# Performance work log

Measured on AMD Instinct MI355X. Metric: run time of the kernel, lower is better.

## Reference

```python
import jax, jax.numpy as jnp
import numpy as np

N_BISECT_ITERS = 50  # entmax library default


def entmax_bisect(X, alpha, n_iter=N_BISECT_ITERS):
    """alpha-entmax over last axis via bisection (Peters & Martins 2019).
    Solves for tau s.t. sum(max((alpha-1)X - tau, 0)^(1/(alpha-1))) = 1."""
    am1 = alpha - 1.0
    inv = 1.0 / am1
    Xa = X * am1
    max_val = jnp.max(Xa, axis=-1, keepdims=True)
    d = X.shape[-1]
    tau_lo = max_val - 1.0                                   # _gp(1, alpha) = 1
    tau_hi = max_val - jnp.asarray(1.0 / d, X.dtype) ** am1  # _gp(1/d, alpha)

    def pfun(tau):
        return jnp.maximum(Xa - tau, 0.0) ** inv

    f_lo = jnp.sum(pfun(tau_lo), axis=-1, keepdims=True) - 1.0

    def body(i, carry):
        tau_lo, dm = carry
        dm = dm * 0.5
        tau_m = tau_lo + dm
        f_m = jnp.sum(pfun(tau_m), axis=-1, keepdims=True) - 1.0
        tau_lo = jnp.where(f_m * f_lo >= 0, tau_m, tau_lo)
        return (tau_lo, dm)

    tau_lo, _ = jax.lax.fori_loop(0, n_iter, body, (tau_lo, tau_hi - tau_lo))
    p = pfun(tau_lo)
    return p / jnp.sum(p, axis=-1, keepdims=True)  # ensure_sum_one


def setup_inputs() -> dict:
    master = jax.random.key(0)
    kq, kk, kv = jax.random.split(master, 3)
    B, H, S, D = 4, 16, 2048, 64
    return {
        "query": jax.random.normal(kq, (B, H, S, D), jnp.float32),
        "key": jax.random.normal(kk, (B, H, S, D), jnp.float32),
        "value": jax.random.normal(kv, (B, H, S, D), jnp.float32),
        "alpha": jnp.float32(1.5),  # canonical entmax-1.5
    }


def reference(query, key, value, alpha):
    D = query.shape[-1]
    scale = 1.0 / jnp.sqrt(jnp.asarray(D, query.dtype))
    scores = jnp.einsum('bhqd,bhkd->bhqk', query, key) * scale  # [B,H,S,S]
    p_attn = entmax_bisect(scores, alpha)
    out = jnp.einsum('bhqk,bhkd->bhqd', p_attn, value)
    return (out, p_attn)
```

## Files before the change

### kernel.cpp

```cpp
#include <hip/hip_runtime.h>
#include <math.h>

#define S_LEN 2048
#define HD    64
#define QT    16
#define NT    1024
#define NW    16
#define NTIL  8
#define CAP   512
#define NITER 28
#define NEWT  10

typedef short s8v __attribute__((ext_vector_type(8)));
typedef float f4v __attribute__((ext_vector_type(4)));

template <bool B> struct BoolT { static constexpr bool value = B; };

__device__ __forceinline__ float wave_sum(float v) {
#pragma unroll
    for (int off = 32; off >= 1; off >>= 1)
        v += __shfl_xor(v, off, 64);
    return v;
}

__device__ __forceinline__ float group16_max(float v) {
#pragma unroll
    for (int off = 8; off >= 1; off >>= 1)
        v = fmaxf(v, __shfl_xor(v, off, 64));
    return v;
}

__device__ __forceinline__ unsigned f2bf2(float lo, float hi) {
    unsigned a = __float_as_uint(lo), b = __float_as_uint(hi);
    a += 0x7FFFu + ((a >> 16) & 1u);
    b += 0x7FFFu + ((b >> 16) & 1u);
    return (a >> 16) | (b & 0xFFFF0000u);
}

__device__ __forceinline__ s8v pack_bf8(const float4& x, const float4& y, float sc) {
    union { s8v s; unsigned u[4]; } f;
    f.u[0] = f2bf2(x.x * sc, x.y * sc);
    f.u[1] = f2bf2(x.z * sc, x.w * sc);
    f.u[2] = f2bf2(y.x * sc, y.y * sc);
    f.u[3] = f2bf2(y.z * sc, y.w * sc);
    return f.s;
}

template <bool INV2>
__device__ __forceinline__ float pfun_t(float t, float inv) {
    float u = fmaxf(t, 0.0f);
    return INV2 ? u * u : powf(u, inv);
}

template <int NR>
__device__ __forceinline__ void newton_reg(const float* cvrow, int ncp, int lane,
                                           float tau0, float& tau_out, float& isum_out) {
    float c[NR];
#pragma unroll
    for (int j = 0; j < NR; ++j) {
        int i = lane + 64 * j;
        c[j] = (i < ncp) ? cvrow[i] : -3.0e38f;
    }
    float tau = tau0;
#pragma unroll
    for (int it = 0; it < NEWT; ++it) {
        float s1 = 0.0f, s2 = 0.0f;
#pragma unroll
        for (int j = 0; j < NR; ++j) {
            float u = fmaxf(c[j] - tau, 0.0f);
            s1 += u;
            s2 = fmaf(u, u, s2);
        }
#pragma unroll
        for (int off = 32; off >= 1; off >>= 1) {
            s1 += __shfl_xor(s1, off, 64);
            s2 += __shfl_xor(s2, off, 64);
        }
        tau += (s2 - 1.0f) * 0.5f * __builtin_amdgcn_rcpf(fmaxf(s1, 1e-30f));
    }
    float s = 0.0f;
#pragma unroll
    for (int j = 0; j < NR; ++j) {
        float u = fmaxf(c[j] - tau, 0.0f);
        s = fmaf(u, u, s);
    }
    s = wave_sum(s);
    tau_out = tau;
    isum_out = 1.0f / s;
}

template <int NR, bool INV2>
__device__ __forceinline__ void bisect_reg(const float* cvrow, int ncp, int lane,
                                           float tau_lo0, float tau_hi, float inv,
                                           float& tau_out, float& isum_out) {
    float c[NR];
#pragma unroll
    for (int j = 0; j < NR; ++j) {
        int i = lane + 64 * j;
        c[j] = (i < ncp) ? cvrow[i] : -3.0e38f;
    }
    float tau = tau_lo0;
    float s0 = 0.0f;
#pragma unroll
    for (int j = 0; j < NR; ++j) s0 += pfun_t<INV2>(c[j] - tau, inv);
    const float f_lo = wave_sum(s0) - 1.0f;
    float dm = tau_hi - tau_lo0;
    for (int it = 0; it < NITER; ++it) {
        dm *= 0.5f;
        float tm = tau + dm;
        float s = 0.0f;
#pragma unroll
        for (int j = 0; j < NR; ++j) s += pfun_t<INV2>(c[j] - tm, inv);
        float fm = wave_sum(s) - 1.0f;
        if (fm * f_lo >= 0.0f) tau = tm;
    }
    float s = 0.0f;
#pragma unroll
    for (int j = 0; j < NR; ++j) s += pfun_t<INV2>(c[j] - tau, inv);
    float ssum = wave_sum(s);
    tau_out = tau;
    isum_out = 1.0f / ssum;
}

__global__ __launch_bounds__(256)
void pack_k(const float* __restrict__ Kp, s8v* __restrict__ Kb) {
    const int idx  = blockIdx.x * 256 + threadIdx.x;
    const int lane = idx & 63;
    const int frag = (idx >> 6) & 1;
    const int tile = (idx >> 7) & (S_LEN / 16 - 1);
    const int bh   = idx >> 14;
    const int l16  = lane & 15, quad = lane >> 4;
    const int row  = tile * 16 + l16;
    const int d0   = frag * 32 + quad * 8;
    const float* src = Kp + ((size_t)bh * S_LEN + row) * HD + d0;
    float4 a = *(const float4*)src;
    float4 b = *(const float4*)(src + 4);
    Kb[idx] = pack_bf8(a, b, 1.0f);
}

template <bool PREK>
__global__ __launch_bounds__(NT)
void entmax_attn(const float* __restrict__ Qp, const float* __restrict__ Kp,
                 const float* __restrict__ Vp, const float* __restrict__ alphap,
                 float* __restrict__ outp, float* __restrict__ pattn,
                 const s8v* __restrict__ Kbf) {
    __shared__ float          candv[QT][CAP];
    __shared__ unsigned short candi[QT][CAP];
    __shared__ int            ncnt[QT];
    __shared__ float          rmaxw[QT][NW];
    __shared__ float          rmxf[QT];
    __shared__ float          taus[QT];
    __shared__ float          isums[QT];
    __shared__ float          redw[NW];

    const int tid   = threadIdx.x;
    const int wv    = tid >> 6;
    const int lane  = tid & 63;
    const int quad  = lane >> 4;
    const int l16   = lane & 15;
    const int bh    = blockIdx.y;
    const int q0    = blockIdx.x * QT;
    const int wcol0 = wv * (NTIL * 16);

    const float alpha = alphap[0];
    const float am1   = alpha - 1.0f;
    const float inv   = 1.0f / am1;
    const bool  inv2  = (inv == 2.0f);
    const float xscale = (1.0f / sqrtf((float)HD)) * am1;
    const float gp_d   = powf(1.0f / (float)S_LEN, am1);

    if (tid < QT) ncnt[tid] = 0;

    const float* kbase = Kp + (size_t)bh * S_LEN * HD;
    const float* vbase = Vp + (size_t)bh * S_LEN * HD;

    s8v qa0, qa1;
    {
        const float* qp = Qp + ((size_t)bh * S_LEN + q0 + l16) * HD + quad * 8;
        float4 x0 = *(const float4*)qp;
        float4 x1 = *(const float4*)(qp + 4);
        float4 y0 = *(const float4*)(qp + 32);
        float4 y1 = *(const float4*)(qp + 36);
        qa0 = pack_bf8(x0, x1, xscale);
        qa1 = pack_bf8(y0, y1, xscale);
    }

    f4v xa[NTIL];
    if constexpr (PREK) {
        const s8v* kf = Kbf + ((size_t)bh * (S_LEN / 16) + (wcol0 >> 4)) * 2 * 64 + lane;
#pragma unroll
        for (int t = 0; t < NTIL; ++t) {
            s8v kb0 = kf[(2 * t    ) * 64];
            s8v kb1 = kf[(2 * t + 1) * 64];
            f4v acc = {0.0f, 0.0f, 0.0f, 0.0f};
            acc = __builtin_amdgcn_mfma_f32_16x16x32_bf16(qa0, kb0, acc, 0, 0, 0);
            acc = __builtin_amdgcn_mfma_f32_16x16x32_bf16(qa1, kb1, acc, 0, 0, 0);
            xa[t] = acc;
        }
    } else {
#pragma unroll
        for (int t = 0; t < NTIL; ++t) {
            const float* kp = kbase + ((size_t)(wcol0 + t * 16 + l16)) * HD + quad * 8;
            float4 k0 = *(const float4*)kp;
            float4 k1 = *(const float4*)(kp + 4);
            s8v kb0 = pack_bf8(k0, k1, 1.0f);
            f4v acc = {0.0f, 0.0f, 0.0f, 0.0f};
            acc = __builtin_amdgcn_mfma_f32_16x16x32_bf16(qa0, kb0, acc, 0, 0, 0);
            float4 k2 = *(const float4*)(kp + 32);
            float4 k3 = *(const float4*)(kp + 36);
            s8v kb1 = pack_bf8(k2, k3, 1.0f);
            acc = __builtin_amdgcn_mfma_f32_16x16x32_bf16(qa1, kb1, acc, 0, 0, 0);
            xa[t] = acc;
        }
    }

#pragma unroll
    for (int g = 0; g < 4; ++g) {
        float pm = xa[0][g];
#pragma unroll
        for (int t = 1; t < NTIL; ++t) pm = fmaxf(pm, xa[t][g]);
        pm = group16_max(pm);
        if (l16 == 0) rmaxw[quad * 4 + g][wv] = pm;
    }
    __syncthreads();
    if (tid < QT) {
        float m = rmaxw[tid][0];
#pragma unroll
        for (int w = 1; w < NW; ++w) m = fmaxf(m, rmaxw[tid][w]);
        rmxf[tid] = m;
    }
    __syncthreads();

    float tl0g[4];
#pragma unroll
    for (int g = 0; g < 4; ++g) tl0g[g] = rmxf[quad * 4 + g] - 1.0f;

#pragma unroll
    for (int t = 0; t < NTIL; ++t) {
#pragma unroll
        for (int g = 0; g < 4; ++g) {
            const float v = xa[t][g];
            const int row = quad * 4 + g;
            const bool pred = (v > tl0g[g]);
            unsigned long long m = __ballot(pred);
            unsigned gm16 = (unsigned)((m >> (quad * 16)) & 0xFFFFull);
            int base = 0;
            if (l16 == 0) {
                int cnt = __popc(gm16);
                if (cnt) base = atomicAdd(&ncnt[row], cnt);
            }
            base = __shfl(base, quad * 16, 64);
            if (pred) {
                int pos = base + __popc(gm16 & ((1u << l16) - 1u));
                if (pos < CAP) {
                    candv[row][pos] = v;
                    candi[row][pos] = (unsigned short)(wcol0 + t * 16 + l16);
                }
            }
        }
    }
    __syncthreads();

    auto tail = [&](auto inv2c) {
        constexpr bool INV2 = decltype(inv2c)::value;

        {
            const int row = wv;
            const int nc = ncnt[row];
            if (nc <= CAP) {
                const int ncp = (nc + 7) & ~7;
                for (int i = nc + lane; i < ncp; i += 64) {
                    candv[row][i] = -3.0e38f;
                    candi[row][i] = 0;
                }
                const float mx  = rmxf[row];
                const float tl0 = mx - 1.0f;
                const float th  = mx - gp_d;
                float tau, isum;
                if constexpr (INV2) {
                    if (ncp <= 256) newton_reg<4>(&candv[row][0], ncp, lane, tl0, tau, isum);
                    else            newton_reg<8>(&candv[row][0], ncp, lane, tl0, tau, isum);
                } else {
                    if (ncp <= 256) bisect_reg<4, INV2>(&candv[row][0], ncp, lane, tl0, th, inv, tau, isum);
                    else            bisect_reg<8, INV2>(&candv[row][0], ncp, lane, tl0, th, inv, tau, isum);
                }
                if (lane == 0) { taus[row] = tau; isums[row] = isum; }
            }
        }

#pragma unroll 1
        for (int r = 0; r < QT; ++r) {
            if (ncnt[r] > CAP) {
                const float mx = rmxf[r];
                const int g = r & 3;
                const bool mine = (quad == (r >> 2));
                float tau = mx - 1.0f;
                float s0 = 0.0f;
                if (mine) {
#pragma unroll
                    for (int t = 0; t < NTIL; ++t) s0 += pfun_t<INV2>(xa[t][g] - tau, inv);
                }
                s0 = wave_sum(s0);
                if (lane == 0) redw[wv] = s0;
                __syncthreads();
                float f_lo = -1.0f;
                for (int w = 0; w < NW; ++w) f_lo += redw[w];
                __syncthreads();
                float dm = (mx - gp_d) - tau;
                for (int it = 0; it < NITER; ++it) {
                    dm *= 0.5f;
                    float tm = tau + dm;
                    float s = 0.0f;
                    if (mine) {
#pragma unroll
                        for (int t = 0; t < NTIL; ++t) s += pfun_t<INV2>(xa[t][g] - tm, inv);
                    }
                    s = wave_sum(s);
                    if (lane == 0) redw[wv] = s;
                    __syncthreads();
                    float fm = -1.0f;
                    for (int w = 0; w < NW; ++w) fm += redw[w];
                    __syncthreads();
                    if (fm * f_lo >= 0.0f) tau = tm;
                }
                float s = 0.0f;
                if (mine) {
#pragma unroll
                    for (int t = 0; t < NTIL; ++t) s += pfun_t<INV2>(xa[t][g] - tau, inv);
                }
                s = wave_sum(s);
                if (lane == 0) redw[wv] = s;
                __syncthreads();
                float ssum = 0.0f;
                for (int w = 0; w < NW; ++w) ssum += redw[w];
                __syncthreads();
                if (tid == 0) { taus[r] = tau; isums[r] = 1.0f / ssum; }
            }
        }
        __syncthreads();

        const size_t prow_base = ((size_t)bh * S_LEN + q0) * S_LEN;
#pragma unroll
        for (int g = 0; g < 4; ++g) {
            const int row = quad * 4 + g;
            const float tau  = taus[row];
            const float isum = isums[row];
            float* prow = pattn + prow_base + (size_t)row * S_LEN + wcol0 + l16;
#pragma unroll
            for (int t = 0; t < NTIL; ++t) {
                prow[t * 16] = pfun_t<INV2>(xa[t][g] - tau, inv) * isum;
            }
        }
        __threadfence_block();
        __syncthreads();

        {
            const int row  = wv;
            const int qrow = q0 + row;
            const int nc   = ncnt[row];
            const float tau  = taus[row];
            const float isum = isums[row];
            float oacc = 0.0f;
            if (nc <= CAP) {
                const int ncp = (nc + 7) & ~7;
                for (int i = lane; i < ncp; i += 64)
                    candv[row][i] = pfun_t<INV2>(candv[row][i] - tau, inv);
                float oacc1 = 0.0f;
                for (int i = 0; i < ncp; i += 8) {
#pragma unroll
                    for (int u = 0; u < 8; u += 2) {
                        oacc  = fmaf(candv[row][i + u],
                                     vbase[(size_t)candi[row][i + u] * HD + lane], oacc);
                        oacc1 = fmaf(candv[row][i + u + 1],
                                     vbase[(size_t)candi[row][i + u + 1] * HD + lane], oacc1);
                    }
                }
                oacc = (oacc + oacc1) * isum;
            } else {
                const float* prow = pattn + ((size_t)bh * S_LEN + qrow) * S_LEN;
                for (int k = 0; k < S_LEN; ++k)
                    oacc = fmaf(prow[k], vbase[(size_t)k * HD + lane], oacc);
            }
            outp[((size_t)bh * S_LEN + qrow) * HD + lane] = oacc;
        }
    };

    if (inv2) tail(BoolT<true>{});
    else      tail(BoolT<false>{});
}

extern "C" void kernel_launch(void* const* d_in, const int* in_sizes, int n_in,
                              void* d_out, int out_size, void* d_ws, size_t ws_size,
                              hipStream_t stream) {
    const float* Q = (const float*)d_in[0];
    const float* K = (const float*)d_in[1];
    const float* V = (const float*)d_in[2];
    const float* A = (const float*)d_in[3];
    float* out = (float*)d_out;
    const int BH = in_sizes[0] / (S_LEN * HD);
    float* p = out + (size_t)BH * S_LEN * HD;
    dim3 grid(S_LEN / QT, BH);

    const size_t kb_bytes = (size_t)BH * S_LEN * HD * sizeof(short);
    if (d_ws != nullptr && ws_size >= kb_bytes) {
        s8v* Kb = (s8v*)d_ws;
        const int nchunk = BH * (S_LEN / 16) * 2 * 64;
        pack_k<<<dim3(nchunk / 256), 256, 0, stream>>>(K, Kb);
        entmax_attn<true><<<grid, NT, 0, stream>>>(Q, K, V, A, out, p, Kb);
    } else {
        entmax_attn<false><<<grid, NT, 0, stream>>>(Q, K, V, A, out, p, nullptr);
    }
}
```

Before: 2.230 ms.

## Compute P·V with bf16 MFMA over pre-packed V fragments instead of sparse gather

Adds a V packing pass that writes bf16 MFMA B-fragments alongside packed K, and a kernel variant that writes squared entmax weights as bf16 into swizzled shared memory, then multiplies against V with MFMA and reduces per-wave partials across the block. This replaces the per-row sparse candidate gather with scalar FMAs and dependent global loads. It hard-codes the alpha=1.5 (square) form in the new path, needs twice the workspace, and lowers P·V precision to bf16.

```diff
diff --git a/kernel.cpp b/kernel.cpp
--- a/kernel.cpp
+++ b/kernel.cpp
@@ -37,6 +37,12 @@
     return (a >> 16) | (b & 0xFFFF0000u);
 }
 
+__device__ __forceinline__ unsigned short f2bf1(float x) {
+    unsigned a = __float_as_uint(x);
+    a += 0x7FFFu + ((a >> 16) & 1u);
+    return (unsigned short)(a >> 16);
+}
+
 __device__ __forceinline__ s8v pack_bf8(const float4& x, const float4& y, float sc) {
     union { s8v s; unsigned u[4]; } f;
     f.u[0] = f2bf2(x.x * sc, x.y * sc);
@@ -123,35 +129,48 @@
 }
 
 __global__ __launch_bounds__(256)
-void pack_k(const float* __restrict__ Kp, s8v* __restrict__ Kb) {
-    const int idx  = blockIdx.x * 256 + threadIdx.x;
-    const int lane = idx & 63;
-    const int frag = (idx >> 6) & 1;
-    const int tile = (idx >> 7) & (S_LEN / 16 - 1);
-    const int bh   = idx >> 14;
-    const int l16  = lane & 15, quad = lane >> 4;
-    const int row  = tile * 16 + l16;
-    const int d0   = frag * 32 + quad * 8;
-    const float* src = Kp + ((size_t)bh * S_LEN + row) * HD + d0;
-    float4 a = *(const float4*)src;
-    float4 b = *(const float4*)(src + 4);
-    Kb[idx] = pack_bf8(a, b, 1.0f);
-}
-
-template <bool PREK>
+void pack_kv(const float* __restrict__ Kp, const float* __restrict__ Vp,
+             s8v* __restrict__ Kb, s8v* __restrict__ Vb, int nK) {
+    int idx = blockIdx.x * 256 + threadIdx.x;
+    if (idx < nK) {
+        const int lane = idx & 63, frag = (idx >> 6) & 1, tile = (idx >> 7) & 127, bh = idx >> 14;
+        const int l16 = lane & 15, quad = lane >> 4;
+        const float* src = Kp + ((size_t)(bh * S_LEN + tile * 16 + l16)) * HD + frag * 32 + quad * 8;
+        float4 a = *(const float4*)src;
+        float4 b = *(const float4*)(src + 4);
+        Kb[idx] = pack_bf8(a, b, 1.0f);
+    } else {
+        int v = idx - nK;
+        const int lane = v & 63, dt = (v >> 6) & 3, ktg = (v >> 8) & 63, bh = v >> 14;
+        const int l16 = lane & 15, quad = lane >> 4;
+        const float* src = Vp + ((size_t)(bh * S_LEN + ktg * 32 + quad * 8)) * HD + dt * 16 + l16;
+        float w[8];
+#pragma unroll
+        for (int j = 0; j < 8; ++j) w[j] = src[(size_t)j * HD];
+        float4 a = {w[0], w[1], w[2], w[3]};
+        float4 b = {w[4], w[5], w[6], w[7]};
+        Vb[v] = pack_bf8(a, b, 1.0f);
+    }
+}
+
+template <bool PREK, bool DPV>
 __global__ __launch_bounds__(NT)
 void entmax_attn(const float* __restrict__ Qp, const float* __restrict__ Kp,
                  const float* __restrict__ Vp, const float* __restrict__ alphap,
                  float* __restrict__ outp, float* __restrict__ pattn,
-                 const s8v* __restrict__ Kbf) {
-    __shared__ float          candv[QT][CAP];
-    __shared__ unsigned short candi[QT][CAP];
-    __shared__ int            ncnt[QT];
-    __shared__ float          rmaxw[QT][NW];
-    __shared__ float          rmxf[QT];
-    __shared__ float          taus[QT];
-    __shared__ float          isums[QT];
-    __shared__ float          redw[NW];
+                 const s8v* __restrict__ Kbf, const s8v* __restrict__ Vbf) {
+    constexpr int SM_BIG = DPV ? (NW * QT * 68 * 4)
+                               : (QT * CAP * 4 + QT * CAP * 2);
+    __shared__ __align__(16) char smem[SM_BIG];
+    float          (*candv)[CAP] = (float(*)[CAP])smem;
+    unsigned short (*candi)[CAP] = (unsigned short(*)[CAP])(smem + QT * CAP * 4);
+
+    __shared__ int   ncnt[QT];
+    __shared__ float rmaxw[QT][NW];
+    __shared__ float rmxf[QT];
+    __shared__ float taus[QT];
+    __shared__ float isums[QT];
+    __shared__ float redw[NW];
 
     const int tid   = threadIdx.x;
     const int wv    = tid >> 6;
@@ -171,7 +190,6 @@
 
     if (tid < QT) ncnt[tid] = 0;
 
-    const float* kbase = Kp + (size_t)bh * S_LEN * HD;
     const float* vbase = Vp + (size_t)bh * S_LEN * HD;
 
     s8v qa0, qa1;
@@ -198,6 +216,7 @@
             xa[t] = acc;
         }
     } else {
+        const float* kbase = Kp + (size_t)bh * S_LEN * HD;
 #pragma unroll
         for (int t = 0; t < NTIL; ++t) {
             const float* kp = kbase + ((size_t)(wcol0 + t * 16 + l16)) * HD + quad * 8;
@@ -254,7 +273,7 @@
                 int pos = base + __popc(gm16 & ((1u << l16) - 1u));
                 if (pos < CAP) {
                     candv[row][pos] = v;
-                    candi[row][pos] = (unsigned short)(wcol0 + t * 16 + l16);
+                    if constexpr (!DPV) candi[row][pos] = (unsigned short)(wcol0 + t * 16 + l16);
                 }
             }
         }
@@ -271,7 +290,7 @@
                 const int ncp = (nc + 7) & ~7;
                 for (int i = nc + lane; i < ncp; i += 64) {
                     candv[row][i] = -3.0e38f;
-                    candi[row][i] = 0;
+                    if constexpr (!DPV) candi[row][i] = 0;
                 }
                 const float mx  = rmxf[row];
                 const float tl0 = mx - 1.0f;
@@ -339,22 +358,73 @@
         }
         __syncthreads();
 
-        const size_t prow_base = ((size_t)bh * S_LEN + q0) * S_LEN;
-#pragma unroll
-        for (int g = 0; g < 4; ++g) {
-            const int row = quad * 4 + g;
-            const float tau  = taus[row];
-            const float isum = isums[row];
-            float* prow = pattn + prow_base + (size_t)row * S_LEN + wcol0 + l16;
-#pragma unroll
-            for (int t = 0; t < NTIL; ++t) {
-                prow[t * 16] = pfun_t<INV2>(xa[t][g] - tau, inv) * isum;
-            }
-        }
-        __threadfence_block();
-        __syncthreads();
-
-        {
+        if constexpr (DPV) {
+            unsigned short* pwf = (unsigned short*)smem + wv * 2048;
+            const size_t prow_base = ((size_t)bh * S_LEN + q0) * S_LEN;
+#pragma unroll
+            for (int g = 0; g < 4; ++g) {
+                const int row = quad * 4 + g;
+                const float tau  = taus[row];
+                const float isum = isums[row];
+                float* prow = pattn + prow_base + (size_t)row * S_LEN + wcol0 + l16;
+#pragma unroll
+                for (int t = 0; t < NTIL; ++t) {
+                    float uu = fmaxf(xa[t][g] - tau, 0.0f);
+                    float p2 = uu * uu;
+                    prow[t * 16] = p2 * isum;
+                    const int col   = t * 16 + l16;
+                    const int slot  = ((col >> 3) ^ row) & 15;
+                    pwf[row * 128 + slot * 8 + (col & 7)] = f2bf1(p2);
+                }
+            }
+            s8v afrag[4];
+#pragma unroll
+            for (int kt = 0; kt < 4; ++kt) {
+                const int slot = ((kt * 4 + quad) ^ l16) & 15;
+                afrag[kt] = *(const s8v*)&pwf[l16 * 128 + slot * 8];
+            }
+            const s8v* vf = Vbf + ((size_t)bh * (S_LEN / 32) + (wcol0 >> 5)) * 4 * 64 + lane;
+            f4v oacc[4];
+#pragma unroll
+            for (int dt = 0; dt < 4; ++dt) oacc[dt] = (f4v){0.0f, 0.0f, 0.0f, 0.0f};
+#pragma unroll
+            for (int kt = 0; kt < 4; ++kt) {
+#pragma unroll
+                for (int dt = 0; dt < 4; ++dt) {
+                    s8v b = vf[(kt * 4 + dt) * 64];
+                    oacc[dt] = __builtin_amdgcn_mfma_f32_16x16x32_bf16(afrag[kt], b, oacc[dt], 0, 0, 0);
+                }
+            }
+            __syncthreads();
+            float* part = (float*)smem;
+#pragma unroll
+            for (int dt = 0; dt < 4; ++dt) {
+#pragma unroll
+                for (int g = 0; g < 4; ++g) {
+                    part[wv * (QT * 68) + (quad * 4 + g) * 68 + dt * 16 + l16] = oacc[dt][g];
+                }
+            }
+            __syncthreads();
+            float s = 0.0f;
+#pragma unroll
+            for (int w = 0; w < NW; ++w) s += part[w * (QT * 68) + wv * 68 + lane];
+            outp[((size_t)bh * S_LEN + q0 + wv) * HD + lane] = s * isums[wv];
+        } else {
+            const size_t prow_base = ((size_t)bh * S_LEN + q0) * S_LEN;
+#pragma unroll
+            for (int g = 0; g < 4; ++g) {
+                const int row = quad * 4 + g;
+                const float tau  = taus[row];
+                const float isum = isums[row];
+                float* prow = pattn + prow_base + (size_t)row * S_LEN + wcol0 + l16;
+#pragma unroll
+                for (int t = 0; t < NTIL; ++t) {
+                    prow[t * 16] = pfun_t<INV2>(xa[t][g] - tau, inv) * isum;
+                }
+            }
+            __threadfence_block();
+            __syncthreads();
+
             const int row  = wv;
             const int qrow = q0 + row;
             const int nc   = ncnt[row];
@@ -402,12 +472,19 @@
     dim3 grid(S_LEN / QT, BH);
 
     const size_t kb_bytes = (size_t)BH * S_LEN * HD * sizeof(short);
-    if (d_ws != nullptr && ws_size >= kb_bytes) {
+    const int nK = BH * (S_LEN / 16) * 2 * 64;
+    const int nV = BH * (S_LEN / 32) * 4 * 64;
+
+    if (d_ws != nullptr && ws_size >= 2 * kb_bytes) {
         s8v* Kb = (s8v*)d_ws;
-        const int nchunk = BH * (S_LEN / 16) * 2 * 64;
-        pack_k<<<dim3(nchunk / 256), 256, 0, stream>>>(K, Kb);
-        entmax_attn<true><<<grid, NT, 0, stream>>>(Q, K, V, A, out, p, Kb);
+        s8v* Vb = (s8v*)((char*)d_ws + kb_bytes);
+        pack_kv<<<dim3((nK + nV) / 256), 256, 0, stream>>>(K, V, Kb, Vb, nK);
+        entmax_attn<true, true><<<grid, NT, 0, stream>>>(Q, K, V, A, out, p, Kb, Vb);
+    } else if (d_ws != nullptr && ws_size >= kb_bytes) {
+        s8v* Kb = (s8v*)d_ws;
+        pack_kv<<<dim3(nK / 256), 256, 0, stream>>>(K, V, Kb, nullptr, nK);
+        entmax_attn<true, false><<<grid, NT, 0, stream>>>(Q, K, V, A, out, p, Kb, nullptr);
     } else {
-        entmax_attn<false><<<grid, NT, 0, stream>>>(Q, K, V, A, out, p, nullptr);
-    }
-}
+        entmax_attn<false, false><<<grid, NT, 0, stream>>>(Q, K, V, A, out, p, nullptr, nullptr);
+    }
+}
```

Result: faster. 1.943 ms (-12.9%).
